# Performance work log

Measured on AMD Instinct MI355X. Metric: run time of the kernel, lower is better.

## Reference

```python
import jax, jax.numpy as jnp
import numpy as np

# --- model dims (from init args) ---
LAYERS = 6
LEAF = 2 ** (LAYERS - 1)        # 32
M_LEN = 128
CAM_NUM = 2
MAIN_CAM = 0
LATENT = 48
H_LAT = 2048                    # LatentNet hidden
H_BR = 512                      # ChooseBranchNet hidden
B = 16384

# Path bits: for leaf i, bit at classifier depth d (root->leaf order) is
# (i >> (LAYERS-2-d)) & 1. This is exactly what the search_table + double
# advanced-indexing gather in the torch code computes (heap tree routing).
_BITS = ((np.arange(LEAF)[:, None] >> np.arange(LAYERS - 2, -1, -1)[None, :]) & 1)  # [LEAF, LAYERS-1]
BITS = jnp.asarray(_BITS, dtype=jnp.int32)


def setup_inputs() -> dict:
    key = jax.random.key(0)
    ks = jax.random.split(key, 9)
    s = lambda fan: 1.0 / np.sqrt(fan)
    return {
        "batch_data": jax.random.normal(ks[0], (B, CAM_NUM, M_LEN), dtype=jnp.float32),
        # LatentNet: [B, 2*M_LEN] -> hidden -> LEAF*LATENT
        "Wl1": jax.random.normal(ks[1], (2 * M_LEN, H_LAT), dtype=jnp.float32) * s(2 * M_LEN),
        "bl1": jnp.zeros((H_LAT,), dtype=jnp.float32),
        "Wl2": jax.random.normal(ks[2], (H_LAT, LEAF * LATENT), dtype=jnp.float32) * s(H_LAT),
        "bl2": jnp.zeros((LEAF * LATENT,), dtype=jnp.float32),
        # ChooseBranchNet (shared across the LAYERS-1 classifier slots): M_LEN -> hidden -> 2
        "Wb1": jax.random.normal(ks[3], (M_LEN, H_BR), dtype=jnp.float32) * s(M_LEN),
        "bb1": jnp.zeros((H_BR,), dtype=jnp.float32),
        "Wb2": jax.random.normal(ks[4], (H_BR, 2), dtype=jnp.float32) * s(H_BR),
        "bb2": jnp.zeros((2,), dtype=jnp.float32),
    }


def reference(batch_data, Wl1, bl1, Wl2, bl2, Wb1, bb1, Wb2, bb2):
    bsz = batch_data.shape[0]
    # expand_measurements: main cam repeated (LAYERS-1) times -> [B, LAYERS-1, M_LEN]
    main = batch_data[:, MAIN_CAM]                                  # [B, M_LEN]
    x_br = jnp.broadcast_to(main[:, None, :], (bsz, LAYERS - 1, M_LEN))
    # ChooseBranchNet -> per-layer 2-way probabilities
    h = jax.nn.relu(jnp.einsum('blm,mh->blh', x_br, Wb1) + bb1)
    p = jax.nn.softmax(jnp.einsum('blh,ho->blo', h, Wb2) + bb2, axis=-1)  # [B, L-1, 2]
    # Tree gates: product of path-branch probabilities along root->leaf path.
    comp = jnp.where(BITS[None] == 1, p[:, None, :, 1], p[:, None, :, 0])  # [B, LEAF, L-1]
    gates = jnp.prod(comp, axis=-1)                                        # [B, LEAF]
    # top-1 routing (argsort(...)[:, -1] as in the torch code)
    router = jnp.argsort(gates, axis=-1)[:, -1]                            # [B]
    # LatentNet on concatenated two-camera measurements
    x2 = jnp.concatenate([batch_data[:, 0], batch_data[:, 1]], axis=-1)    # [B, 2*M_LEN]
    hl = jax.nn.relu(x2 @ Wl1 + bl1)
    nn_latent = (hl @ Wl2 + bl2).reshape(bsz, LEAF, LATENT)
    # scatter-select per-sample leaf latent (replaces the torch.where loop)
    select = jnp.take_along_axis(nn_latent, router[:, None, None], axis=1)[:, 0]  # [B, LATENT]
    return select
```

## Files before the change

### kernel.cpp

```cpp
#include <hip/hip_runtime.h>
#include <stdint.h>

typedef short bf16x8 __attribute__((ext_vector_type(8)));
typedef float f32x4 __attribute__((ext_vector_type(4)));

#define NROWS 16384
#define NSLOTS 16448
#define K1DIM 256
#define N1DIM 2048
#define MARGIN 0.03f

#define GLD16(g, l) __builtin_amdgcn_global_load_lds( \
    (const __attribute__((address_space(1))) uint32_t*)(g), \
    (__attribute__((address_space(3))) uint32_t*)(l), 16, 0, 0)

__device__ __forceinline__ ushort f2bf(float x) {
  union { float f; uint32_t u; } c; c.f = x;
  uint32_t u = c.u;
  return (ushort)((u + 0x7FFFu + ((u >> 16) & 1u)) >> 16);
}

__global__ __launch_bounds__(256) void k0_convert(
    const float* __restrict__ bd, const float* __restrict__ Wl1,
    const float* __restrict__ Wl2, const float* __restrict__ Wb1,
    ushort* __restrict__ x2bf, ushort* __restrict__ wl1t,
    ushort* __restrict__ w2t, ushort* __restrict__ wb1t) {
  int i = blockIdx.x * 256 + threadIdx.x;
  {
    float4 v = ((const float4*)bd)[i];
    ushort4 o;
    o.x = f2bf(v.x); o.y = f2bf(v.y); o.z = f2bf(v.z); o.w = f2bf(v.w);
    ((ushort4*)x2bf)[i] = o;
  }
  if (i < 2048 * 256) {
    int n = i >> 8, k = i & 255;
    wl1t[i] = f2bf(Wl1[k * 2048 + n]);
  }
  if (i < 96 * 2048) {
    int j = i >> 11, k = i & 2047;
    int col = (j < 48) ? j : (1440 + j);
    w2t[i] = f2bf(Wl2[k * 1536 + col]);
  }
  if (i < 512 * 128) {
    int j = i >> 7, m = i & 127;
    wb1t[i] = f2bf(Wb1[m * 512 + j]);
  }
}

__global__ __launch_bounds__(256) void k1a_score(
    const ushort* __restrict__ x2bf, const ushort* __restrict__ wb1t,
    const float* __restrict__ bb1, const float* __restrict__ Wb2,
    float* __restrict__ part) {
  __shared__ __align__(1024) ushort As[128 * 64];
  __shared__ __align__(1024) ushort Bs[128 * 64];
  const int t = threadIdx.x, ln = t & 63, wv = t >> 6;
  const int m0 = blockIdx.y << 7;
  const int n0 = blockIdx.x << 7;
  const int wm = (wv >> 1) << 6, wn = (wv & 1) << 6;
  const int rsub = ln >> 3, kc8 = ln & 7;
  const int q = ln >> 4, rr = ln & 15;

  f32x4 acc[4][4] = {};

  for (int k0 = 0; k0 < 128; k0 += 64) {
#pragma unroll
    for (int i = 0; i < 4; i++) {
      int inst = (wv << 2) + i;
      int row = (inst << 3) + rsub;
      GLD16(x2bf + (size_t)(m0 + row) * 256 + k0 + (kc8 << 3), As + (inst << 9));
      GLD16(wb1t + (size_t)(n0 + row) * 128 + k0 + (kc8 << 3), Bs + (inst << 9));
    }
    __syncthreads();
#pragma unroll
    for (int kk = 0; kk < 2; kk++) {
      int kb = ((kk << 2) + q) << 3;
      bf16x8 af[4], bfr[4];
#pragma unroll
      for (int mi = 0; mi < 4; mi++)
        af[mi] = *(const bf16x8*)(As + (((wm + (mi << 4) + rr)) << 6) + kb);
#pragma unroll
      for (int ni = 0; ni < 4; ni++)
        bfr[ni] = *(const bf16x8*)(Bs + (((wn + (ni << 4) + rr)) << 6) + kb);
#pragma unroll
      for (int mi = 0; mi < 4; mi++)
#pragma unroll
        for (int ni = 0; ni < 4; ni++)
          acc[mi][ni] = __builtin_amdgcn_mfma_f32_16x16x32_bf16(
              af[mi], bfr[ni], acc[mi][ni], 0, 0, 0);
    }
    __syncthreads();
  }

  float s4[4][4] = {};
#pragma unroll
  for (int ni = 0; ni < 4; ni++) {
    int col = n0 + wn + (ni << 4) + rr;
    float bias = bb1[col];
    float wdv = Wb2[col * 2 + 1] - Wb2[col * 2];
#pragma unroll
    for (int mi = 0; mi < 4; mi++) {
      f32x4 a = acc[mi][ni];
#pragma unroll
      for (int v = 0; v < 4; v++)
        s4[mi][v] += fmaxf(a[v] + bias, 0.f) * wdv;
    }
  }
#pragma unroll
  for (int off = 1; off <= 8; off <<= 1)
#pragma unroll
    for (int mi = 0; mi < 4; mi++)
#pragma unroll
      for (int v = 0; v < 4; v++)
        s4[mi][v] += __shfl_xor(s4[mi][v], off);

  if (rr == 0) {
    float* dst = part + (size_t)(blockIdx.x * 2 + (wv & 1)) * NROWS +
                 m0 + wm + (q << 2);
#pragma unroll
    for (int mi = 0; mi < 4; mi++) {
      float4 v4 = make_float4(s4[mi][0], s4[mi][1], s4[mi][2], s4[mi][3]);
      *(float4*)(dst + (mi << 4)) = v4;
    }
  }
}

__global__ __launch_bounds__(256) void k1b_classify(
    const float* __restrict__ part, const float* __restrict__ bb2,
    int* __restrict__ router, int* __restrict__ list, int* __restrict__ counters) {
  int t = blockIdx.x * 256 + threadIdx.x;
  float s = bb2[1] - bb2[0];
#pragma unroll
  for (int i = 0; i < 8; i++) s += part[i * NROWS + t];
  router[t] = (s >= 0.f) ? 1 : 0;
  if (fabsf(s) < MARGIN) {
    int idx = atomicAdd(&counters[0], 1);
    list[idx] = t;
  }
}

__global__ __launch_bounds__(256) void k1c_recheck(
    const float* __restrict__ bd, const float* __restrict__ Wb1,
    const float* __restrict__ Wb2, const float* __restrict__ bb1,
    const float* __restrict__ bb2, const int* __restrict__ list,
    const int* __restrict__ counters, int* __restrict__ router) {
  const int ln = threadIdx.x & 63;
  const int wid = (blockIdx.x * 256 + threadIdx.x) >> 6;
  const int count = counters[0];
  const float c = bb2[1] - bb2[0];

  for (int base = wid * 4; base < count; base += 512 * 4) {
    int rows[4];
#pragma unroll
    for (int r = 0; r < 4; r++) {
      int idx = base + r;
      rows[r] = list[(idx < count) ? idx : base];
    }
    float acc[4][8];
#pragma unroll
    for (int r = 0; r < 4; r++)
#pragma unroll
      for (int u = 0; u < 8; u++) acc[r][u] = 0.f;

    for (int m = 0; m < 128; m++) {
      float w[8];
#pragma unroll
      for (int u = 0; u < 8; u++) w[u] = Wb1[m * 512 + (u << 6) + ln];
#pragma unroll
      for (int r = 0; r < 4; r++) {
        float x = bd[(size_t)rows[r] * 256 + m];
#pragma unroll
        for (int u = 0; u < 8; u++) acc[r][u] = fmaf(x, w[u], acc[r][u]);
      }
    }
    float sc[4];
#pragma unroll
    for (int r = 0; r < 4; r++) {
      float s = 0.f;
#pragma unroll
      for (int u = 0; u < 8; u++) {
        int j = (u << 6) + ln;
        float wd = Wb2[j * 2 + 1] - Wb2[j * 2];
        s += fmaxf(acc[r][u] + bb1[j], 0.f) * wd;
      }
#pragma unroll
      for (int off = 1; off <= 32; off <<= 1) s += __shfl_xor(s, off);
      sc[r] = s + c;
    }
    if (ln == 0) {
#pragma unroll
      for (int r = 0; r < 4; r++)
        if (base + r < count) router[rows[r]] = (sc[r] >= 0.f) ? 1 : 0;
    }
  }
}

__global__ __launch_bounds__(256) void k1d_rowmap(
    const int* __restrict__ router, int* __restrict__ rowmap,
    int* __restrict__ counters) {
  int t = blockIdx.x * 256 + threadIdx.x;
  int sel = router[t];
  int slot = sel ? (NSLOTS - 1 - atomicAdd(&counters[2], 1))
                 : atomicAdd(&counters[1], 1);
  rowmap[slot] = t;
}

__global__ __launch_bounds__(256, 3) void k2_fused(
    const ushort* __restrict__ x2bf, const ushort* __restrict__ wl1t,
    const ushort* __restrict__ w2t, const float* __restrict__ bl1,
    const float* __restrict__ bl2, const int* __restrict__ rowmap,
    const int* __restrict__ counters, float* __restrict__ out) {
  __shared__ __align__(1024) ushort As[4096];
  __shared__ __align__(1024) ushort WtHs[16384];
  __shared__ __align__(1024) ushort Ws[6144];
  ushort* Wt = WtHs;
  ushort* Hs = WtHs;
  const int t = threadIdx.x, ln = t & 63, wv = t >> 6;
  const int ks2 = blockIdx.x;
  const int m0 = blockIdx.y << 6;
  const int q = ln >> 4, rr = ln & 15;
  const int r8 = ln >> 3, s8 = ln & 7;
  const int r4 = ln >> 4, s16 = ln & 15;
  const int c0 = counters[1];
  const int sel_blk = (m0 >= c0) ? 1 : 0;
  const int selbase = sel_blk * 48;

  int g_as[2];
#pragma unroll
  for (int ii = 0; ii < 2; ii++) {
    int g = rowmap[m0 + (((wv << 1) + ii) << 3) + r8];
    g_as[ii] = (g < 0) ? 0 : g;
  }

  f32x4 accP[3] = {};

  for (int nc = 0; nc < 4; nc++) {
    const int n0 = (ks2 << 10) + (nc << 8);

    f32x4 acc1[4][4] = {};
#pragma unroll 1
    for (int ks = 0; ks < 4; ks++) {
      const int kg = ks << 6;
#pragma unroll
      for (int ii = 0; ii < 2; ii++)
        GLD16(x2bf + (size_t)g_as[ii] * 256 + kg + ((s8 ^ r8) << 3),
              As + ((((wv << 1) + ii)) << 9));
#pragma unroll
      for (int ii = 0; ii < 8; ii++) {
        int inst = (wv << 3) + ii;
        int r = (inst << 3) + r8;
        GLD16(wl1t + (size_t)(n0 + r) * 256 + kg + ((s8 ^ r8) << 3),
              Wt + (inst << 9));
      }
      __syncthreads();
#pragma unroll
      for (int kk = 0; kk < 2; kk++) {
        int c = (kk << 2) + q;
        int sl = (c ^ (rr & 7)) << 3;
        bf16x8 af[4], bfv[4];
#pragma unroll
        for (int mi = 0; mi < 4; mi++)
          af[mi] = *(const bf16x8*)(Wt + (((wv << 6) + (mi << 4) + rr) << 6) + sl);
#pragma unroll
        for (int ni = 0; ni < 4; ni++)
          bfv[ni] = *(const bf16x8*)(As + (((ni << 4) + rr) << 6) + sl);
#pragma unroll
        for (int mi = 0; mi < 4; mi++)
#pragma unroll
          for (int ni = 0; ni < 4; ni++)
            acc1[mi][ni] = __builtin_amdgcn_mfma_f32_16x16x32_bf16(
                af[mi], bfv[ni], acc1[mi][ni], 0, 0, 0);
      }
      __syncthreads();
    }

#pragma unroll
    for (int mi = 0; mi < 4; mi++) {
      int p = (wv << 4) + (mi << 2) + q;
      float bias0 = bl1[n0 + (p << 2) + 0];
      float bias1 = bl1[n0 + (p << 2) + 1];
      float bias2 = bl1[n0 + (p << 2) + 2];
      float bias3 = bl1[n0 + (p << 2) + 3];
#pragma unroll
      for (int ni = 0; ni < 4; ni++) {
        int hsrow = (ni << 4) + rr;
        f32x4 a = acc1[mi][ni];
        ushort4 pk;
        pk.x = f2bf(fmaxf(a[0] + bias0, 0.f));
        pk.y = f2bf(fmaxf(a[1] + bias1, 0.f));
        pk.z = f2bf(fmaxf(a[2] + bias2, 0.f));
        pk.w = f2bf(fmaxf(a[3] + bias3, 0.f));
        *(ushort4*)(Hs + (hsrow << 8) + ((p ^ rr) << 2)) = pk;
      }
    }

#pragma unroll 1
    for (int h = 0; h < 2; h++) {
#pragma unroll
      for (int jj = 0; jj < 3; jj++) {
        int inst = wv * 3 + jj;
        int r = (inst << 2) + r4;
        int c = s16 ^ (r & 15);
        GLD16(w2t + (size_t)(selbase + r) * 2048 + n0 + (h << 7) + (c << 3),
              Ws + (inst << 9));
      }
      __syncthreads();
#pragma unroll
      for (int kk = 0; kk < 4; kk++) {
        int p0 = (h << 5) + (kk << 3) + (q << 1);
        int hrow = (wv << 4) + rr;
        union { ushort4 u[2]; bf16x8 v; } hu;
        hu.u[0] = *(const ushort4*)(Hs + (hrow << 8) + ((p0 ^ rr) << 2));
        hu.u[1] = *(const ushort4*)(Hs + (hrow << 8) + (((p0 + 1) ^ rr) << 2));
        int c = (kk << 2) + q;
#pragma unroll
        for (int ni = 0; ni < 3; ni++) {
          bf16x8 wb = *(const bf16x8*)(Ws + (((ni << 4) + rr) << 7) +
                                       ((c ^ rr) << 3));
          accP[ni] = __builtin_amdgcn_mfma_f32_16x16x32_bf16(
              hu.v, wb, accP[ni], 0, 0, 0);
        }
      }
      __syncthreads();
    }
  }

  {
    float b[3] = {0.f, 0.f, 0.f};
    if (ks2 == 0) {
#pragma unroll
      for (int ni = 0; ni < 3; ni++)
        b[ni] = bl2[sel_blk * 1488 + (ni << 4) + rr];
    }
#pragma unroll
    for (int v = 0; v < 4; v++) {
      int slot = m0 + (wv << 4) + (q << 2) + v;
      int orig = rowmap[slot];
      if (orig >= 0) {
        float* ob = out + (size_t)orig * 48 + rr;
        atomicAdd(ob, accP[0][v] + b[0]);
        atomicAdd(ob + 16, accP[1][v] + b[1]);
        atomicAdd(ob + 32, accP[2][v] + b[2]);
      }
    }
  }
}

extern "C" void kernel_launch(void* const* d_in, const int* in_sizes, int n_in,
                              void* d_out, int out_size, void* d_ws, size_t ws_size,
                              hipStream_t stream) {
  const float* bd  = (const float*)d_in[0];
  const float* Wl1 = (const float*)d_in[1];
  const float* bl1 = (const float*)d_in[2];
  const float* Wl2 = (const float*)d_in[3];
  const float* bl2 = (const float*)d_in[4];
  const float* Wb1 = (const float*)d_in[5];
  const float* bb1 = (const float*)d_in[6];
  const float* Wb2 = (const float*)d_in[7];
  const float* bb2 = (const float*)d_in[8];

  char* ws = (char*)d_ws;
  ushort* x2bf  = (ushort*)(ws);
  ushort* wl1t  = (ushort*)(ws + 8388608);
  ushort* w2t   = (ushort*)(ws + 9437184);
  int*    router= (int*)(ws + 89522176);
  ushort* wb1t  = (ushort*)(ws + 89587712);
  float*  part  = (float*)(ws + 89718784);
  int*    list  = (int*)(ws + 90243072);
  int*    counters=(int*)(ws + 90308608);
  int*    rowmap= (int*)(ws + 90310656);
  float*  outp  = (float*)d_out;

  k0_convert<<<dim3(4096), dim3(256), 0, stream>>>(bd, Wl1, Wl2, Wb1,
                                                   x2bf, wl1t, w2t, wb1t);
  hipMemsetAsync(counters, 0, 12, stream);
  hipMemsetAsync(rowmap, 0xFF, NSLOTS * 4, stream);
  hipMemsetAsync(outp, 0, (size_t)out_size * 4, stream);
  k1a_score<<<dim3(4, 128), dim3(256), 0, stream>>>(x2bf, wb1t, bb1, Wb2, part);
  k1b_classify<<<dim3(64), dim3(256), 0, stream>>>(part, bb2, router, list,
                                                   counters);
  k1c_recheck<<<dim3(128), dim3(256), 0, stream>>>(bd, Wb1, Wb2, bb1, bb2,
                                                   list, counters, router);
  k1d_rowmap<<<dim3(64), dim3(256), 0, stream>>>(router, rowmap, counters);
  k2_fused<<<dim3(2, 257), dim3(256), 0, stream>>>(x2bf, wl1t, w2t, bl1, bl2,
                                                   rowmap, counters, outp);
}
```

Baseline: 180.0 us.

## Fuse router scoring, margin recheck and rowmap into one split-bf16 kernel

```diff
diff --git a/kernel.cpp b/kernel.cpp
--- a/kernel.cpp
+++ b/kernel.cpp
@@ -7,8 +7,7 @@
 #define NROWS 16384
 #define NSLOTS 16448
 #define K1DIM 256
-#define N1DIM 2048
-#define MARGIN 0.03f
+#define MARGIN2 2e-3f
 
 #define GLD16(g, l) __builtin_amdgcn_global_load_lds( \
     (const __attribute__((address_space(1))) uint32_t*)(g), \
@@ -19,12 +18,19 @@
   uint32_t u = c.u;
   return (ushort)((u + 0x7FFFu + ((u >> 16) & 1u)) >> 16);
 }
+__device__ __forceinline__ float bf2f(ushort h) {
+  union { float f; uint32_t u; } c; c.u = ((uint32_t)h) << 16;
+  return c.f;
+}
 
 __global__ __launch_bounds__(256) void k0_convert(
     const float* __restrict__ bd, const float* __restrict__ Wl1,
     const float* __restrict__ Wl2, const float* __restrict__ Wb1,
     ushort* __restrict__ x2bf, ushort* __restrict__ wl1t,
-    ushort* __restrict__ w2t, ushort* __restrict__ wb1t) {
+    ushort* __restrict__ w2t, ushort* __restrict__ wb1t,
+    ushort* __restrict__ wb1lo, ushort* __restrict__ x1lo,
+    int* __restrict__ rowmap, int* __restrict__ counters,
+    float* __restrict__ out) {
   int i = blockIdx.x * 256 + threadIdx.x;
   {
     float4 v = ((const float4*)bd)[i];
@@ -32,6 +38,15 @@
     o.x = f2bf(v.x); o.y = f2bf(v.y); o.z = f2bf(v.z); o.w = f2bf(v.w);
     ((ushort4*)x2bf)[i] = o;
   }
+  if (i < 524288) {
+    int r = i >> 5, c = i & 31;
+    float4 v = ((const float4*)bd)[(r << 6) + c];
+    ushort4 h, l;
+    h.x = f2bf(v.x); h.y = f2bf(v.y); h.z = f2bf(v.z); h.w = f2bf(v.w);
+    l.x = f2bf(v.x - bf2f(h.x)); l.y = f2bf(v.y - bf2f(h.y));
+    l.z = f2bf(v.z - bf2f(h.z)); l.w = f2bf(v.w - bf2f(h.w));
+    ((ushort4*)x1lo)[i] = l;
+  }
   if (i < 2048 * 256) {
     int n = i >> 8, k = i & 255;
     wl1t[i] = f2bf(Wl1[k * 2048 + n]);
@@ -43,68 +58,113 @@
   }
   if (i < 512 * 128) {
     int j = i >> 7, m = i & 127;
-    wb1t[i] = f2bf(Wb1[m * 512 + j]);
-  }
-}
-
-__global__ __launch_bounds__(256) void k1a_score(
-    const ushort* __restrict__ x2bf, const ushort* __restrict__ wb1t,
-    const float* __restrict__ bb1, const float* __restrict__ Wb2,
-    float* __restrict__ part) {
-  __shared__ __align__(1024) ushort As[128 * 64];
-  __shared__ __align__(1024) ushort Bs[128 * 64];
+    float w = Wb1[m * 512 + j];
+    ushort h = f2bf(w);
+    wb1t[i] = h;
+    wb1lo[i] = f2bf(w - bf2f(h));
+  }
+  if (i < 196608) ((float4*)out)[i] = make_float4(0.f, 0.f, 0.f, 0.f);
+  if (i < NSLOTS) rowmap[i] = -1;
+  if (i < 8) counters[i] = 0;
+}
+
+__global__ __launch_bounds__(256) void k1_router(
+    const ushort* __restrict__ x2bf, const ushort* __restrict__ x1lo,
+    const ushort* __restrict__ wb1t, const ushort* __restrict__ wb1lo,
+    const float* __restrict__ bd, const float* __restrict__ Wb1,
+    const float* __restrict__ Wb2, const float* __restrict__ bb1,
+    const float* __restrict__ bb2, int* __restrict__ rowmap,
+    int* __restrict__ counters) {
+  __shared__ __align__(1024) ushort Xh[64 * 128];
+  __shared__ __align__(1024) ushort Xl[64 * 128];
+  __shared__ __align__(1024) ushort Wh[128 * 128];
+  __shared__ __align__(1024) ushort Wl[128 * 128];
+  __shared__ float red[256];
+  __shared__ float scores[64];
+  __shared__ float redw[4];
+  __shared__ int mlist[64];
+  __shared__ int nmarg;
   const int t = threadIdx.x, ln = t & 63, wv = t >> 6;
-  const int m0 = blockIdx.y << 7;
-  const int n0 = blockIdx.x << 7;
-  const int wm = (wv >> 1) << 6, wn = (wv & 1) << 6;
-  const int rsub = ln >> 3, kc8 = ln & 7;
+  const int m0 = blockIdx.x << 6;
   const int q = ln >> 4, rr = ln & 15;
 
-  f32x4 acc[4][4] = {};
-
-  for (int k0 = 0; k0 < 128; k0 += 64) {
-#pragma unroll
-    for (int i = 0; i < 4; i++) {
-      int inst = (wv << 2) + i;
-      int row = (inst << 3) + rsub;
-      GLD16(x2bf + (size_t)(m0 + row) * 256 + k0 + (kc8 << 3), As + (inst << 9));
-      GLD16(wb1t + (size_t)(n0 + row) * 128 + k0 + (kc8 << 3), Bs + (inst << 9));
+  if (t == 0) nmarg = 0;
+
+#pragma unroll
+  for (int ii = 0; ii < 4; ii++) {
+    int inst = (wv << 2) + ii;
+    int r = (inst << 2) + q;
+    int sl = (rr ^ (r & 15)) << 3;
+    GLD16(x2bf + (size_t)(m0 + r) * 256 + sl, Xh + (inst << 9));
+    GLD16(x1lo + (size_t)(m0 + r) * 128 + sl, Xl + (inst << 9));
+  }
+
+  float s4[4][4];
+#pragma unroll
+  for (int a = 0; a < 4; a++)
+#pragma unroll
+    for (int b = 0; b < 4; b++) s4[a][b] = 0.f;
+
+  for (int nc = 0; nc < 4; nc++) {
+#pragma unroll
+    for (int ii = 0; ii < 8; ii++) {
+      int inst = (wv << 3) + ii;
+      int jr = (inst << 2) + q;
+      int jg = (nc << 7) + jr;
+      int sl = (rr ^ (jr & 15)) << 3;
+      GLD16(wb1t + (size_t)jg * 128 + sl, Wh + (inst << 9));
+      GLD16(wb1lo + (size_t)jg * 128 + sl, Wl + (inst << 9));
     }
     __syncthreads();
-#pragma unroll
-    for (int kk = 0; kk < 2; kk++) {
-      int kb = ((kk << 2) + q) << 3;
-      bf16x8 af[4], bfr[4];
+
+    f32x4 acc[4][2] = {};
+#pragma unroll
+    for (int kk = 0; kk < 4; kk++) {
+      int c = (kk << 2) + q;
+      bf16x8 xh[4], xl[4], wh[2], wlv[2];
+#pragma unroll
+      for (int mi = 0; mi < 4; mi++) {
+        int row = (mi << 4) + rr;
+        int sl = (c ^ rr) << 3;
+        xh[mi] = *(const bf16x8*)(Xh + (row << 7) + sl);
+        xl[mi] = *(const bf16x8*)(Xl + (row << 7) + sl);
+      }
+#pragma unroll
+      for (int ni = 0; ni < 2; ni++) {
+        int row = (wv << 5) + (ni << 4) + rr;
+        int sl = (c ^ rr) << 3;
+        wh[ni] = *(const bf16x8*)(Wh + (row << 7) + sl);
+        wlv[ni] = *(const bf16x8*)(Wl + (row << 7) + sl);
+      }
 #pragma unroll
       for (int mi = 0; mi < 4; mi++)
-        af[mi] = *(const bf16x8*)(As + (((wm + (mi << 4) + rr)) << 6) + kb);
-#pragma unroll
-      for (int ni = 0; ni < 4; ni++)
-        bfr[ni] = *(const bf16x8*)(Bs + (((wn + (ni << 4) + rr)) << 6) + kb);
-#pragma unroll
-      for (int mi = 0; mi < 4; mi++)
-#pragma unroll
-        for (int ni = 0; ni < 4; ni++)
+#pragma unroll
+        for (int ni = 0; ni < 2; ni++) {
           acc[mi][ni] = __builtin_amdgcn_mfma_f32_16x16x32_bf16(
-              af[mi], bfr[ni], acc[mi][ni], 0, 0, 0);
+              xh[mi], wh[ni], acc[mi][ni], 0, 0, 0);
+          acc[mi][ni] = __builtin_amdgcn_mfma_f32_16x16x32_bf16(
+              xh[mi], wlv[ni], acc[mi][ni], 0, 0, 0);
+          acc[mi][ni] = __builtin_amdgcn_mfma_f32_16x16x32_bf16(
+              xl[mi], wh[ni], acc[mi][ni], 0, 0, 0);
+        }
     }
     __syncthreads();
-  }
-
-  float s4[4][4] = {};
-#pragma unroll
-  for (int ni = 0; ni < 4; ni++) {
-    int col = n0 + wn + (ni << 4) + rr;
-    float bias = bb1[col];
-    float wdv = Wb2[col * 2 + 1] - Wb2[col * 2];
-#pragma unroll
-    for (int mi = 0; mi < 4; mi++) {
-      f32x4 a = acc[mi][ni];
-#pragma unroll
-      for (int v = 0; v < 4; v++)
-        s4[mi][v] += fmaxf(a[v] + bias, 0.f) * wdv;
-    }
-  }
+
+#pragma unroll
+    for (int ni = 0; ni < 2; ni++) {
+      int j = (nc << 7) + (wv << 5) + (ni << 4) + rr;
+      float bias = bb1[j];
+      float wd = Wb2[j * 2 + 1] - Wb2[j * 2];
+#pragma unroll
+      for (int mi = 0; mi < 4; mi++) {
+        f32x4 a = acc[mi][ni];
+#pragma unroll
+        for (int v = 0; v < 4; v++)
+          s4[mi][v] += fmaxf(a[v] + bias, 0.f) * wd;
+      }
+    }
+  }
+
 #pragma unroll
   for (int off = 1; off <= 8; off <<= 1)
 #pragma unroll
@@ -112,96 +172,53 @@
 #pragma unroll
       for (int v = 0; v < 4; v++)
         s4[mi][v] += __shfl_xor(s4[mi][v], off);
-
   if (rr == 0) {
-    float* dst = part + (size_t)(blockIdx.x * 2 + (wv & 1)) * NROWS +
-                 m0 + wm + (q << 2);
-#pragma unroll
-    for (int mi = 0; mi < 4; mi++) {
-      float4 v4 = make_float4(s4[mi][0], s4[mi][1], s4[mi][2], s4[mi][3]);
-      *(float4*)(dst + (mi << 4)) = v4;
-    }
-  }
-}
-
-__global__ __launch_bounds__(256) void k1b_classify(
-    const float* __restrict__ part, const float* __restrict__ bb2,
-    int* __restrict__ router, int* __restrict__ list, int* __restrict__ counters) {
-  int t = blockIdx.x * 256 + threadIdx.x;
-  float s = bb2[1] - bb2[0];
-#pragma unroll
-  for (int i = 0; i < 8; i++) s += part[i * NROWS + t];
-  router[t] = (s >= 0.f) ? 1 : 0;
-  if (fabsf(s) < MARGIN) {
-    int idx = atomicAdd(&counters[0], 1);
-    list[idx] = t;
-  }
-}
-
-__global__ __launch_bounds__(256) void k1c_recheck(
-    const float* __restrict__ bd, const float* __restrict__ Wb1,
-    const float* __restrict__ Wb2, const float* __restrict__ bb1,
-    const float* __restrict__ bb2, const int* __restrict__ list,
-    const int* __restrict__ counters, int* __restrict__ router) {
-  const int ln = threadIdx.x & 63;
-  const int wid = (blockIdx.x * 256 + threadIdx.x) >> 6;
-  const int count = counters[0];
-  const float c = bb2[1] - bb2[0];
-
-  for (int base = wid * 4; base < count; base += 512 * 4) {
-    int rows[4];
-#pragma unroll
-    for (int r = 0; r < 4; r++) {
-      int idx = base + r;
-      rows[r] = list[(idx < count) ? idx : base];
-    }
-    float acc[4][8];
-#pragma unroll
-    for (int r = 0; r < 4; r++)
-#pragma unroll
-      for (int u = 0; u < 8; u++) acc[r][u] = 0.f;
-
+#pragma unroll
+    for (int mi = 0; mi < 4; mi++)
+#pragma unroll
+      for (int v = 0; v < 4; v++)
+        red[(wv << 6) + (mi << 4) + (q << 2) + v] = s4[mi][v];
+  }
+  __syncthreads();
+
+  const float cdiff = bb2[1] - bb2[0];
+  if (t < 64) {
+    float s = red[t] + red[64 + t] + red[128 + t] + red[192 + t] + cdiff;
+    scores[t] = s;
+    if (fabsf(s) < MARGIN2) {
+      int idx = atomicAdd(&nmarg, 1);
+      mlist[idx] = t;
+    }
+  }
+  __syncthreads();
+
+  int nm = nmarg;
+  for (int i = 0; i < nm; i++) {
+    int row = mlist[i];
+    float a0 = 0.f, a1 = 0.f;
+    int j0 = t << 1;
+    const float* xr = bd + (size_t)(m0 + row) * 256;
     for (int m = 0; m < 128; m++) {
-      float w[8];
-#pragma unroll
-      for (int u = 0; u < 8; u++) w[u] = Wb1[m * 512 + (u << 6) + ln];
-#pragma unroll
-      for (int r = 0; r < 4; r++) {
-        float x = bd[(size_t)rows[r] * 256 + m];
-#pragma unroll
-        for (int u = 0; u < 8; u++) acc[r][u] = fmaf(x, w[u], acc[r][u]);
-      }
-    }
-    float sc[4];
-#pragma unroll
-    for (int r = 0; r < 4; r++) {
-      float s = 0.f;
-#pragma unroll
-      for (int u = 0; u < 8; u++) {
-        int j = (u << 6) + ln;
-        float wd = Wb2[j * 2 + 1] - Wb2[j * 2];
-        s += fmaxf(acc[r][u] + bb1[j], 0.f) * wd;
-      }
-#pragma unroll
-      for (int off = 1; off <= 32; off <<= 1) s += __shfl_xor(s, off);
-      sc[r] = s + c;
-    }
-    if (ln == 0) {
-#pragma unroll
-      for (int r = 0; r < 4; r++)
-        if (base + r < count) router[rows[r]] = (sc[r] >= 0.f) ? 1 : 0;
-    }
-  }
-}
-
-__global__ __launch_bounds__(256) void k1d_rowmap(
-    const int* __restrict__ router, int* __restrict__ rowmap,
-    int* __restrict__ counters) {
-  int t = blockIdx.x * 256 + threadIdx.x;
-  int sel = router[t];
-  int slot = sel ? (NSLOTS - 1 - atomicAdd(&counters[2], 1))
-                 : atomicAdd(&counters[1], 1);
-  rowmap[slot] = t;
+      float x = xr[m];
+      a0 = fmaf(x, Wb1[m * 512 + j0], a0);
+      a1 = fmaf(x, Wb1[m * 512 + j0 + 1], a1);
+    }
+    float s = fmaxf(a0 + bb1[j0], 0.f) * (Wb2[j0 * 2 + 1] - Wb2[j0 * 2]) +
+              fmaxf(a1 + bb1[j0 + 1], 0.f) * (Wb2[j0 * 2 + 3] - Wb2[j0 * 2 + 2]);
+#pragma unroll
+    for (int off = 1; off <= 32; off <<= 1) s += __shfl_xor(s, off);
+    if (ln == 0) redw[wv] = s;
+    __syncthreads();
+    if (t == 0) scores[row] = redw[0] + redw[1] + redw[2] + redw[3] + cdiff;
+    __syncthreads();
+  }
+
+  if (t < 64) {
+    int sel = (scores[t] >= 0.f) ? 1 : 0;
+    int slot = sel ? (NSLOTS - 1 - atomicAdd(&counters[2], 1))
+                   : atomicAdd(&counters[1], 1);
+    rowmap[slot] = m0 + t;
+  }
 }
 
 __global__ __launch_bounds__(256, 3) void k2_fused(
@@ -362,25 +379,18 @@
   ushort* x2bf  = (ushort*)(ws);
   ushort* wl1t  = (ushort*)(ws + 8388608);
   ushort* w2t   = (ushort*)(ws + 9437184);
-  int*    router= (int*)(ws + 89522176);
-  ushort* wb1t  = (ushort*)(ws + 89587712);
-  float*  part  = (float*)(ws + 89718784);
-  int*    list  = (int*)(ws + 90243072);
-  int*    counters=(int*)(ws + 90308608);
-  int*    rowmap= (int*)(ws + 90310656);
+  ushort* x1lo  = (ushort*)(ws + 9830400);
+  ushort* wb1t  = (ushort*)(ws + 14024704);
+  ushort* wb1lo = (ushort*)(ws + 14155776);
+  int*    rowmap= (int*)(ws + 14286848);
+  int*    counters=(int*)(ws + 14352640);
   float*  outp  = (float*)d_out;
 
-  k0_convert<<<dim3(4096), dim3(256), 0, stream>>>(bd, Wl1, Wl2, Wb1,
-                                                   x2bf, wl1t, w2t, wb1t);
-  hipMemsetAsync(counters, 0, 12, stream);
-  hipMemsetAsync(rowmap, 0xFF, NSLOTS * 4, stream);
-  hipMemsetAsync(outp, 0, (size_t)out_size * 4, stream);
-  k1a_score<<<dim3(4, 128), dim3(256), 0, stream>>>(x2bf, wb1t, bb1, Wb2, part);
-  k1b_classify<<<dim3(64), dim3(256), 0, stream>>>(part, bb2, router, list,
-                                                   counters);
-  k1c_recheck<<<dim3(128), dim3(256), 0, stream>>>(bd, Wb1, Wb2, bb1, bb2,
-                                                   list, counters, router);
-  k1d_rowmap<<<dim3(64), dim3(256), 0, stream>>>(router, rowmap, counters);
-  k2_fused<<<dim3(2, 257), dim3(256), 0, stream>>>(x2bf, wl1t, w2t, bl1, bl2,
-                                                   rowmap, counters, outp);
-}
+  k0_convert<<<dim3(4096), dim3(256), 0, stream>>>(
+      bd, Wl1, Wl2, Wb1, x2bf, wl1t, w2t, wb1t, wb1lo, x1lo,
+      rowmap, counters, outp);
+  k1_router<<<dim3(256), dim3(256), 0, stream>>>(
+      x2bf, x1lo, wb1t, wb1lo, bd, Wb1, Wb2, bb1, bb2, rowmap, counters);
+  k2_fused<<<dim3(2, 257), dim3(256), 0, stream>>>(
+      x2bf, wl1t, w2t, bl1, bl2, rowmap, counters, outp);
+}
```

New measurement: 158.3 us. 1.14x faster.
